# Kernel tuning notes

Hardware: AMD Instinct MI355X
Metric: run time of the kernel (lower is better)

The kernel has to match this reference:

```python
import jax, jax.numpy as jnp
import numpy as np

EPS = 1e-6

def _conv1x1(x, w, b):
    # x: [b,c,h,w], w: [o,c], b: [o] -> per-pixel matmul
    return jnp.einsum('bchw,oc->bohw', x, w) + b[None, :, None, None]

def setup_inputs() -> dict:
    key = jax.random.key(0)
    ks = jax.random.split(key, 10)
    b, c, h, w = 16, 256, 128, 128
    dec = jax.random.normal(ks[0], (b, c, h, w), jnp.float32)
    enc = jax.random.normal(ks[1], (b, c, h, w), jnp.float32)
    ln_w = jnp.ones((c,), jnp.float32)
    ln_b = jnp.zeros((c,), jnp.float32)
    w0 = jax.random.normal(ks[2], (c, c), jnp.float32) * 0.05
    b0 = jax.random.normal(ks[3], (c,), jnp.float32) * 0.05
    w1 = jax.random.normal(ks[4], (c // 2, c), jnp.float32) * 0.05
    b1 = jax.random.normal(ks[5], (c // 2,), jnp.float32) * 0.05
    w2 = jax.random.normal(ks[6], (c // 4, c // 2), jnp.float32) * 0.05
    b2 = jax.random.normal(ks[7], (c // 4,), jnp.float32) * 0.05
    w3 = jax.random.normal(ks[8], (1, c // 4), jnp.float32) * 0.05
    b3 = jax.random.normal(ks[9], (1,), jnp.float32) * 0.05
    return dict(dec=dec, enc=enc, ln_w=ln_w, ln_b=ln_b, w0=w0, b0=b0,
                w1=w1, b1=b1, w2=w2, b2=b2, w3=w3, b3=b3)

def reference(dec, enc, ln_w, ln_b, w0, b0, w1, b1, w2, b2, w3, b3):
    b, c, h, w = dec.shape
    x = dec + enc
    # LayerNorm2d: normalize over channel dim per pixel (biased var, eps=1e-6)
    mu = jnp.mean(x, axis=1, keepdims=True)
    var = jnp.var(x, axis=1, keepdims=True)
    x = (x - mu) / jnp.sqrt(var + EPS) * ln_w[None, :, None, None] + ln_b[None, :, None, None]
    # in_conv: 1x1 conv + exact GELU
    x = jax.nn.gelu(_conv1x1(x, w0, b0), approximate=False)
    # split: local channels kept, global channels pooled and broadcast back
    local_x = x[:, :c // 2]                                   # [b,c/2,h,w]
    global_x = jnp.mean(x[:, c // 2:], axis=(2, 3), keepdims=True)  # [b,c/2,1,1]
    x = jnp.concatenate([local_x, jnp.broadcast_to(global_x, local_x.shape)], axis=1)
    # mask_pre: nc -> nc/2 -> nc/4 -> 1 with GELUs
    x = jax.nn.gelu(_conv1x1(x, w1, b1), approximate=False)
    x = jax.nn.gelu(_conv1x1(x, w2, b2), approximate=False)
    x = _conv1x1(x, w3, b3)
    return jax.nn.sigmoid(x)
```

## Files before the change

kernel.cpp:

```cpp
#include <hip/hip_runtime.h>
#include <math.h>

typedef float f32x4 __attribute__((ext_vector_type(4)));
typedef short s8v __attribute__((ext_vector_type(8)));

#define LN_EPS 1e-6f

static __device__ __forceinline__ unsigned short f2bf(float f) {
  union { float f; unsigned int u; } v; v.f = f;
  unsigned int r = (v.u + 0x7FFFu + ((v.u >> 16) & 1u)) >> 16;
  return (unsigned short)r;
}
static __device__ __forceinline__ float bf2f(unsigned short b) {
  union { float f; unsigned int u; } v; v.u = ((unsigned int)b) << 16;
  return v.f;
}
static __device__ __forceinline__ unsigned int f2bf_pk(float lo, float hi) {
  unsigned int r;
  asm("v_cvt_pk_bf16_f32 %0, %1, %2" : "=v"(r) : "v"(lo), "v"(hi));
  return r;
}
static __device__ __forceinline__ float gelu_fast(float x) {
  float t = x * x;
  float u = x * fmaf(t, 0.07135481283f, 1.5957691216f);
  float e = __expf(-u);
  return __fdividef(x, 1.0f + e);
}

__global__ void prep_kernel(const float* __restrict__ w0, const float* __restrict__ w1,
                            const float* __restrict__ w2, const float* __restrict__ lnw,
                            const float* __restrict__ lnb, const float* __restrict__ b0,
                            unsigned short* __restrict__ wt0f, unsigned short* __restrict__ w1f,
                            unsigned short* __restrict__ w2f, float* __restrict__ gacc,
                            float* __restrict__ sfold, float* __restrict__ tfold) {
  int idx = blockIdx.x * blockDim.x + threadIdx.x;
  int stride = gridDim.x * blockDim.x;
  const int N0 = 65536, N1 = 16384, N2 = 8192, N3 = 2048, N4 = 256;
  for (int i = idx; i < N0 + N1 + N2 + N3 + N4; i += stride) {
    if (i < N0) {
      int j = i & 7, l = (i >> 3) & 63, ks = (i >> 9) & 7, n0 = i >> 12;
      int k = ks * 32 + (l >> 4) * 8 + j;
      wt0f[i] = f2bf(w0[(n0 * 16 + (l & 15)) * 256 + k] * lnw[k]);
    } else if (i < N0 + N1) {
      int t = i - N0;
      int j = t & 7, l = (t >> 3) & 63, ks = (t >> 9) & 3, n0 = t >> 11;
      w1f[t] = f2bf(w1[(n0 * 16 + (l & 15)) * 256 + ks * 32 + (l >> 4) * 8 + j]);
    } else if (i < N0 + N1 + N2) {
      int t = i - N0 - N1;
      int j = t & 7, l = (t >> 3) & 63, ks = (t >> 9) & 3, n0 = t >> 11;
      w2f[t] = f2bf(w2[(n0 * 16 + (l & 15)) * 128 + ks * 32 + (l >> 4) * 8 + j]);
    } else if (i < N0 + N1 + N2 + N3) {
      gacc[i - N0 - N1 - N2] = 0.0f;
    } else {
      int n = i - N0 - N1 - N2 - N3;
      float s = 0.f, t = 0.f;
      for (int c = 0; c < 256; ++c) {
        float wv = w0[n * 256 + c];
        s += wv * lnw[c];
        t += wv * lnb[c];
      }
      sfold[n] = s;
      tfold[n] = t + b0[n];
    }
  }
}


#define ISSUE_Q(dr, er, q)                                                   \
  _Pragma("unroll") for (int s = 0; s < 4; ++s) {                            \
    const int c = (q) * 64 + g4 * 4 + s;                                     \
    dr[s] = *(const f32x4*)(dec + base + (long)c * 16384);                   \
    er[s] = *(const f32x4*)(enc + base + (long)c * 16384);                   \
  }

#define CONVERT_Q(dr, er, q) {                                               \
  f32x4 xv[4];                                                               \
  _Pragma("unroll") for (int s = 0; s < 4; ++s) {                            \
    xv[s] = dr[s] + er[s]; sum += xv[s]; sq += xv[s] * xv[s];                \
  }                                                                          \
  _Pragma("unroll") for (int px = 0; px < 4; ++px) {                         \
    const int p = (kq << 2) + px;                                            \
    uint2 hv;                                                                \
    hv.x = f2bf_pk(xv[0][px], xv[1][px]);                                    \
    hv.y = f2bf_pk(xv[2][px], xv[3][px]);                                    \
    const int byte = (p * 512 + (q) * 128 + g4 * 8) ^ ((p & 7) << 4);        \
    *(uint2*)(&At[byte]) = hv;                                               \
  } }

#define GEMM_Q(q)                                                            \
  _Pragma("unroll") for (int kk = 0; kk < 2; ++kk) {                         \
    const int ks = (q) * 2 + kk;                                             \
    s8v a[4];                                                                \
    _Pragma("unroll") for (int mi = 0; mi < 4; ++mi) {                       \
      const int p = mi * 16 + l15;                                           \
      const int byte = (p * 512 + ks * 64 + lg * 16) ^ ((p & 7) << 4);       \
      a[mi] = *(const s8v*)(&At[byte]);                                      \
    }                                                                        \
    _Pragma("unroll") for (int ni = 0; ni < 4; ++ni) {                       \
      const int n0 = w * 4 + ni;                                             \
      s8v bfr = *(const s8v*)(wt0f + ((n0 * 8 + ks) * 64 + lane) * 8);       \
      _Pragma("unroll") for (int mi = 0; mi < 4; ++mi)                       \
        acc[mi][ni] =                                                        \
            __builtin_amdgcn_mfma_f32_16x16x32_bf16(a[mi], bfr, acc[mi][ni], 0, 0, 0); \
    }                                                                        \
  }

#define LBAR() {                                                             \
  asm volatile("s_waitcnt lgkmcnt(0)" ::: "memory");                         \
  __builtin_amdgcn_s_barrier();                                              \
  __builtin_amdgcn_sched_barrier(0);                                         \
}

__global__ __launch_bounds__(256, 3) void k1_kernel(
    const float* __restrict__ dec, const float* __restrict__ enc,
    const unsigned short* __restrict__ wt0f,
    const float* __restrict__ sfold, const float* __restrict__ tfold,
    unsigned short* __restrict__ yl, float* __restrict__ gacc) {
  __shared__ __align__(16) unsigned char At[64 * 512];
  __shared__ float wred[4][16][8];
  __shared__ float alphaL[64], betaL[64];

  const int tid = threadIdx.x, blk = blockIdx.x;
  const int b = blk >> 8;
  const int hw0 = (blk & 255) << 6;
  const int g4 = tid >> 4, kq = tid & 15;
  const int lane = tid & 63, w = tid >> 6, l15 = lane & 15, lg = lane >> 4;

  const long base = (long)(b * 256) * 16384 + hw0 + (kq << 2);

  f32x4 sum = {0.f, 0.f, 0.f, 0.f}, sq = {0.f, 0.f, 0.f, 0.f};
  f32x4 acc[4][4];
#pragma unroll
  for (int mi = 0; mi < 4; ++mi)
#pragma unroll
    for (int ni = 0; ni < 4; ++ni) acc[mi][ni] = (f32x4){0.f, 0.f, 0.f, 0.f};

  f32x4 d0[4], e0[4], d1[4], e1[4];

  ISSUE_Q(d0, e0, 0);
  ISSUE_Q(d1, e1, 1);

  CONVERT_Q(d0, e0, 0);
  LBAR();
  GEMM_Q(0);
  ISSUE_Q(d0, e0, 2);

  CONVERT_Q(d1, e1, 1);
  LBAR();
  GEMM_Q(1);
  ISSUE_Q(d1, e1, 3);

  CONVERT_Q(d0, e0, 2);
  LBAR();
  GEMM_Q(2);

  CONVERT_Q(d1, e1, 3);

#pragma unroll
  for (int q = 0; q < 4; ++q) {
    sum[q] += __shfl_xor(sum[q], 16, 64);
    sq[q] += __shfl_xor(sq[q], 16, 64);
    sum[q] += __shfl_xor(sum[q], 32, 64);
    sq[q] += __shfl_xor(sq[q], 32, 64);
  }
  if (lane < 16) {
#pragma unroll
    for (int q = 0; q < 4; ++q) { wred[w][lane][q] = sum[q]; wred[w][lane][4 + q] = sq[q]; }
  }
  __syncthreads();

  if (tid < 64) {
    const int kk = tid >> 2, comp = tid & 3;
    float s = 0.f, s2 = 0.f;
#pragma unroll
    for (int ww = 0; ww < 4; ++ww) { s += wred[ww][kk][comp]; s2 += wred[ww][kk][4 + comp]; }
    const float mu = s * (1.0f / 256.0f);
    const float var = s2 * (1.0f / 256.0f) - mu * mu;
    const float rs = rsqrtf(var + LN_EPS);
    alphaL[tid] = rs;
    betaL[tid] = -mu * rs;
  }
  GEMM_Q(3);
  __syncthreads();

  float sn[4], tn[4];
#pragma unroll
  for (int ni = 0; ni < 4; ++ni) {
    const int n = w * 64 + ni * 16 + l15;
    sn[ni] = sfold[n];
    tn[ni] = tfold[n];
  }

  if (w < 2) {
#pragma unroll
    for (int mi = 0; mi < 4; ++mi) {
      const f32x4 al = *(const f32x4*)(&alphaL[mi * 16 + lg * 4]);
      const f32x4 be = *(const f32x4*)(&betaL[mi * 16 + lg * 4]);
#pragma unroll
      for (int r = 0; r < 4; ++r) {
        const int p = mi * 16 + lg * 4 + r;
#pragma unroll
        for (int ni = 0; ni < 4; ++ni) {
          const float v = gelu_fast(fmaf(al[r], acc[mi][ni][r], fmaf(be[r], sn[ni], tn[ni])));
          const int col = w * 64 + ni * 16 + l15;
          const int byte = (p * 256 + col * 2) ^ ((p & 7) << 4);
          *(unsigned short*)(&At[byte]) = f2bf(v);
        }
      }
    }
  } else {
    float ps[4] = {0.f, 0.f, 0.f, 0.f};
#pragma unroll
    for (int mi = 0; mi < 4; ++mi) {
      const f32x4 al = *(const f32x4*)(&alphaL[mi * 16 + lg * 4]);
      const f32x4 be = *(const f32x4*)(&betaL[mi * 16 + lg * 4]);
#pragma unroll
      for (int r = 0; r < 4; ++r) {
#pragma unroll
        for (int ni = 0; ni < 4; ++ni)
          ps[ni] += gelu_fast(fmaf(al[r], acc[mi][ni][r], fmaf(be[r], sn[ni], tn[ni])));
      }
    }
#pragma unroll
    for (int ni = 0; ni < 4; ++ni) {
      float p2 = ps[ni];
      p2 += __shfl_xor(p2, 16, 64);
      p2 += __shfl_xor(p2, 32, 64);
      if (lane < 16) atomicAdd(&gacc[b * 128 + (w - 2) * 64 + ni * 16 + lane], p2);
    }
  }
  __syncthreads();

  {
    const long rowbase = ((long)b * 16384 + hw0);
#pragma unroll
    for (int q = 0; q < 4; ++q) {
      const int p = q * 16 + (tid >> 4);
      const int colb = (tid & 15) * 16;
      const int byte = (p * 256 + colb) ^ ((p & 7) << 4);
      s8v v = *(const s8v*)(&At[byte]);
      __builtin_nontemporal_store(v, (s8v*)((char*)yl + (rowbase + p) * 256 + colb));
    }
  }
}

__global__ void kmid_kernel(const float* __restrict__ w1, const float* __restrict__ b1,
                            const float* __restrict__ gacc, float* __restrict__ g1) {
  int b = blockIdx.x, o = threadIdx.x;
  float acc = b1[o];
  const float inv = 1.0f / 16384.0f;
  for (int c = 0; c < 128; ++c)
    acc += w1[o * 256 + 128 + c] * (gacc[b * 128 + c] * inv);
  g1[b * 128 + o] = acc;
}

__global__ __launch_bounds__(256, 4) void k2_kernel(
    const unsigned short* __restrict__ yl, const float* __restrict__ g1,
    const float* __restrict__ b2v, const float* __restrict__ w3,
    const float* __restrict__ b3, const unsigned short* __restrict__ w1f,
    const unsigned short* __restrict__ w2f, float* __restrict__ out) {
  __shared__ __align__(16) unsigned char Yt[64 * 256];
  __shared__ __align__(16) unsigned char Z1[64 * 256];
  __shared__ __align__(16) unsigned char Z2[64 * 128];
  __shared__ float part3[4][64];
  __shared__ float w3S[64];

  const int tid = threadIdx.x, blk = blockIdx.x;
  const int lane = tid & 63, w = tid >> 6, l15 = lane & 15, lg = lane >> 4;
  const int P0 = blk * 64;
  const int b = blk >> 8;

  if (tid < 64) w3S[tid] = w3[tid];

#pragma unroll
  for (int q = 0; q < 4; ++q) {
    int p = q * 16 + (tid >> 4);
    int c2 = (tid & 15) * 16;
    s8v v = *(const s8v*)((const char*)yl + (long)(P0 + p) * 256 + c2);
    int byte = (p * 256 + c2) ^ ((p & 7) << 4);
    *(s8v*)(&Yt[byte]) = v;
  }
  __syncthreads();

  f32x4 acc1[4][2];
#pragma unroll
  for (int mi = 0; mi < 4; ++mi)
#pragma unroll
    for (int ni = 0; ni < 2; ++ni) acc1[mi][ni] = (f32x4){0.f, 0.f, 0.f, 0.f};
#pragma unroll
  for (int ks = 0; ks < 4; ++ks) {
    s8v a[4];
#pragma unroll
    for (int mi = 0; mi < 4; ++mi) {
      int p = mi * 16 + l15;
      int byte = (p * 256 + ks * 64 + lg * 16) ^ ((p & 7) << 4);
      a[mi] = *(const s8v*)(&Yt[byte]);
    }
#pragma unroll
    for (int ni = 0; ni < 2; ++ni) {
      int n0 = w * 2 + ni;
      s8v bfr = *(const s8v*)(w1f + ((n0 * 4 + ks) * 64 + lane) * 8);
#pragma unroll
      for (int mi = 0; mi < 4; ++mi)
        acc1[mi][ni] = __builtin_amdgcn_mfma_f32_16x16x32_bf16(a[mi], bfr, acc1[mi][ni], 0, 0, 0);
    }
  }
#pragma unroll
  for (int ni = 0; ni < 2; ++ni) {
    int o = (w * 2 + ni) * 16 + l15;
    float bias = g1[b * 128 + o];
#pragma unroll
    for (int mi = 0; mi < 4; ++mi)
#pragma unroll
      for (int r = 0; r < 4; ++r) {
        int p = mi * 16 + lg * 4 + r;
        float v = gelu_fast(acc1[mi][ni][r] + bias);
        int byte = (p * 256 + o * 2) ^ ((p & 7) << 4);
        *(unsigned short*)(&Z1[byte]) = f2bf(v);
      }
  }
  __syncthreads();

  f32x4 acc2[4];
#pragma unroll
  for (int mi = 0; mi < 4; ++mi) acc2[mi] = (f32x4){0.f, 0.f, 0.f, 0.f};
#pragma unroll
  for (int ks = 0; ks < 4; ++ks) {
    s8v a[4];
#pragma unroll
    for (int mi = 0; mi < 4; ++mi) {
      int p = mi * 16 + l15;
      int byte = (p * 256 + ks * 64 + lg * 16) ^ ((p & 7) << 4);
      a[mi] = *(const s8v*)(&Z1[byte]);
    }
    s8v bfr = *(const s8v*)(w2f + ((w * 4 + ks) * 64 + lane) * 8);
#pragma unroll
    for (int mi = 0; mi < 4; ++mi)
      acc2[mi] = __builtin_amdgcn_mfma_f32_16x16x32_bf16(a[mi], bfr, acc2[mi], 0, 0, 0);
  }
  {
    int o = w * 16 + l15;
    float bias = b2v[o];
#pragma unroll
    for (int mi = 0; mi < 4; ++mi)
#pragma unroll
      for (int r = 0; r < 4; ++r) {
        int p = mi * 16 + lg * 4 + r;
        float v = gelu_fast(acc2[mi][r] + bias);
        int byte = (p * 128 + o * 2) ^ ((p & 7) << 4);
        *(unsigned short*)(&Z2[byte]) = f2bf(v);
      }
  }
  __syncthreads();

  {
    int p = tid & 63, cg = tid >> 6;
    float dot = 0.f;
#pragma unroll
    for (int half = 0; half < 2; ++half) {
      int byte = (p * 128 + cg * 32 + half * 16) ^ ((p & 7) << 4);
      s8v z = *(const s8v*)(&Z2[byte]);
#pragma unroll
      for (int j = 0; j < 8; ++j)
        dot += bf2f((unsigned short)z[j]) * w3S[cg * 16 + half * 8 + j];
    }
    part3[cg][p] = dot;
  }
  __syncthreads();
  if (tid < 64) {
    float t = part3[0][tid] + part3[1][tid] + part3[2][tid] + part3[3][tid] + b3[0];
    out[P0 + tid] = __fdividef(1.0f, 1.0f + __expf(-t));
  }
}

extern "C" void kernel_launch(void* const* d_in, const int* in_sizes, int n_in,
                              void* d_out, int out_size, void* d_ws, size_t ws_size,
                              hipStream_t stream) {
  const float* dec = (const float*)d_in[0];
  const float* enc = (const float*)d_in[1];
  const float* lnw = (const float*)d_in[2];
  const float* lnb = (const float*)d_in[3];
  const float* w0  = (const float*)d_in[4];
  const float* b0  = (const float*)d_in[5];
  const float* w1  = (const float*)d_in[6];
  const float* b1  = (const float*)d_in[7];
  const float* w2  = (const float*)d_in[8];
  const float* b2  = (const float*)d_in[9];
  const float* w3  = (const float*)d_in[10];
  const float* b3  = (const float*)d_in[11];

  char* ws = (char*)d_ws;
  unsigned short* yl   = (unsigned short*)ws;
  unsigned short* wt0f = (unsigned short*)(ws + 67108864);
  unsigned short* w1f  = (unsigned short*)(ws + 67239936);
  unsigned short* w2f  = (unsigned short*)(ws + 67272704);
  float* gacc          = (float*)(ws + 67289088);
  float* g1            = (float*)(ws + 67297280);
  float* sfold         = (float*)(ws + 67305472);
  float* tfold         = (float*)(ws + 67306496);

  prep_kernel<<<128, 256, 0, stream>>>(w0, w1, w2, lnw, lnb, b0, wt0f, w1f, w2f,
                                       gacc, sfold, tfold);
  k1_kernel<<<4096, 256, 0, stream>>>(dec, enc, wt0f, sfold, tfold, yl, gacc);
  kmid_kernel<<<16, 128, 0, stream>>>(w1, b1, gacc, g1);
  k2_kernel<<<4096, 256, 0, stream>>>(yl, g1, b2, w3, b3, w1f, w2f, (float*)d_out);
}
```

Baseline: 257.0 us.

## Restructure k1 load/convert/GEMM pipeline from quarters into halves

The first kernel's K loop is restructured from four 64-channel quarters with double-buffered register loads into two 128-channel halves. Each thread now loads 8 channels per half, writes 16-byte LDS stores instead of 8-byte ones, and there are fewer barriers between GEMM phases. Launch bounds drop from 3 to 2 blocks per CU to make room for the larger register footprint. The risk is lower occupancy and less overlap of global loads with MFMA work, since the second half's loads are issued before the first GEMM with a single buffer.

```diff
diff --git a/kernel.cpp b/kernel.cpp
--- a/kernel.cpp
+++ b/kernel.cpp
@@ -3,6 +3,7 @@
 
 typedef float f32x4 __attribute__((ext_vector_type(4)));
 typedef short s8v __attribute__((ext_vector_type(8)));
+typedef unsigned int u32x4 __attribute__((ext_vector_type(4)));
 
 #define LN_EPS 1e-6f
 
@@ -66,30 +67,30 @@
 }
 
 
-#define ISSUE_Q(dr, er, q)                                                   \
-  _Pragma("unroll") for (int s = 0; s < 4; ++s) {                            \
-    const int c = (q) * 64 + g4 * 4 + s;                                     \
+#define ISSUE_H(h)                                                           \
+  _Pragma("unroll") for (int s = 0; s < 8; ++s) {                            \
+    const int c = (h) * 128 + g * 8 + s;                                     \
     dr[s] = *(const f32x4*)(dec + base + (long)c * 16384);                   \
     er[s] = *(const f32x4*)(enc + base + (long)c * 16384);                   \
   }
 
-#define CONVERT_Q(dr, er, q) {                                               \
-  f32x4 xv[4];                                                               \
-  _Pragma("unroll") for (int s = 0; s < 4; ++s) {                            \
+#define CONVERT_H(h) {                                                       \
+  f32x4 xv[8];                                                               \
+  _Pragma("unroll") for (int s = 0; s < 8; ++s) {                            \
     xv[s] = dr[s] + er[s]; sum += xv[s]; sq += xv[s] * xv[s];                \
   }                                                                          \
   _Pragma("unroll") for (int px = 0; px < 4; ++px) {                         \
     const int p = (kq << 2) + px;                                            \
-    uint2 hv;                                                                \
-    hv.x = f2bf_pk(xv[0][px], xv[1][px]);                                    \
-    hv.y = f2bf_pk(xv[2][px], xv[3][px]);                                    \
-    const int byte = (p * 512 + (q) * 128 + g4 * 8) ^ ((p & 7) << 4);        \
-    *(uint2*)(&At[byte]) = hv;                                               \
+    u32x4 hv;                                                                \
+    _Pragma("unroll") for (int sp = 0; sp < 4; ++sp)                         \
+      hv[sp] = f2bf_pk(xv[2 * sp][px], xv[2 * sp + 1][px]);                  \
+    const int byte = (p * 512 + (h) * 256 + g * 16) ^ ((p & 7) << 4);        \
+    *(u32x4*)(&At[byte]) = hv;                                               \
   } }
 
-#define GEMM_Q(q)                                                            \
-  _Pragma("unroll") for (int kk = 0; kk < 2; ++kk) {                         \
-    const int ks = (q) * 2 + kk;                                             \
+#define GEMM_HALF(h)                                                         \
+  _Pragma("unroll") for (int kk = 0; kk < 4; ++kk) {                         \
+    const int ks = (h) * 4 + kk;                                             \
     s8v a[4];                                                                \
     _Pragma("unroll") for (int mi = 0; mi < 4; ++mi) {                       \
       const int p = mi * 16 + l15;                                           \
@@ -111,7 +112,7 @@
   __builtin_amdgcn_sched_barrier(0);                                         \
 }
 
-__global__ __launch_bounds__(256, 3) void k1_kernel(
+__global__ __launch_bounds__(256, 2) void k1_kernel(
     const float* __restrict__ dec, const float* __restrict__ enc,
     const unsigned short* __restrict__ wt0f,
     const float* __restrict__ sfold, const float* __restrict__ tfold,
@@ -123,7 +124,7 @@
   const int tid = threadIdx.x, blk = blockIdx.x;
   const int b = blk >> 8;
   const int hw0 = (blk & 255) << 6;
-  const int g4 = tid >> 4, kq = tid & 15;
+  const int g = tid >> 4, kq = tid & 15;
   const int lane = tid & 63, w = tid >> 6, l15 = lane & 15, lg = lane >> 4;
 
   const long base = (long)(b * 256) * 16384 + hw0 + (kq << 2);
@@ -135,26 +136,14 @@
 #pragma unroll
     for (int ni = 0; ni < 4; ++ni) acc[mi][ni] = (f32x4){0.f, 0.f, 0.f, 0.f};
 
-  f32x4 d0[4], e0[4], d1[4], e1[4];
-
-  ISSUE_Q(d0, e0, 0);
-  ISSUE_Q(d1, e1, 1);
-
-  CONVERT_Q(d0, e0, 0);
+  f32x4 dr[8], er[8];
+
+  ISSUE_H(0);
+  CONVERT_H(0);
+  ISSUE_H(1);
   LBAR();
-  GEMM_Q(0);
-  ISSUE_Q(d0, e0, 2);
-
-  CONVERT_Q(d1, e1, 1);
-  LBAR();
-  GEMM_Q(1);
-  ISSUE_Q(d1, e1, 3);
-
-  CONVERT_Q(d0, e0, 2);
-  LBAR();
-  GEMM_Q(2);
-
-  CONVERT_Q(d1, e1, 3);
+  GEMM_HALF(0);
+  CONVERT_H(1);
 
 #pragma unroll
   for (int q = 0; q < 4; ++q) {
@@ -167,7 +156,7 @@
 #pragma unroll
     for (int q = 0; q < 4; ++q) { wred[w][lane][q] = sum[q]; wred[w][lane][4 + q] = sq[q]; }
   }
-  __syncthreads();
+  LBAR();
 
   if (tid < 64) {
     const int kk = tid >> 2, comp = tid & 3;
@@ -180,7 +169,7 @@
     alphaL[tid] = rs;
     betaL[tid] = -mu * rs;
   }
-  GEMM_Q(3);
+  GEMM_HALF(1);
   __syncthreads();
 
   float sn[4], tn[4];
```

Result: faster. 211.6 us (-17.7%).
